# Performance work log

Hardware: AMD Instinct MI355X
Metric: run time of the kernel (lower is better)

## Reference

```python
import jax, jax.numpy as jnp
import numpy as np

EMBED_PHI = 1024
EMBED_F = 1024
HIDDEN_F = 1024
N_HEADS = 16
B, S = 2, 2048


def setup_inputs() -> dict:
    key = jax.random.key(0)
    ks = jax.random.split(key, 9)
    sphi = 1.0 / np.sqrt(EMBED_PHI)
    sf = 1.0 / np.sqrt(EMBED_F)
    sh = 1.0 / np.sqrt(HIDDEN_F)
    return {
        "q": jax.random.normal(ks[0], (B, S, EMBED_PHI), jnp.float32),
        "k": jax.random.normal(ks[1], (B, S, EMBED_PHI), jnp.float32),
        "v": jax.random.normal(ks[2], (B, S, EMBED_F), jnp.float32),
        "Wq": jax.random.normal(ks[3], (HIDDEN_F, EMBED_PHI), jnp.float32) * sphi,
        "Wk": jax.random.normal(ks[4], (HIDDEN_F, EMBED_PHI), jnp.float32) * sphi,
        "Wv": jax.random.normal(ks[5], (HIDDEN_F, EMBED_F), jnp.float32) * sf,
        "bv": jax.random.normal(ks[6], (HIDDEN_F,), jnp.float32) * sf,
        "Wo": jax.random.normal(ks[7], (EMBED_F, HIDDEN_F), jnp.float32) * sh,
        "bo": jax.random.normal(ks[8], (EMBED_F,), jnp.float32) * sh,
    }


def reference(q, k, v, Wq, Wk, Wv, bv, Wo, bo):
    Bq, Sq, _ = q.shape
    hd = HIDDEN_F // N_HEADS
    scale = 1.0 / np.sqrt(hd)
    # projections; torch Linear: y = x @ W.T + b
    qh = (q @ Wq.T).reshape(Bq, Sq, N_HEADS, hd).transpose(0, 2, 1, 3)  # [B,H,S,d]
    kh = (k @ Wk.T).reshape(Bq, Sq, N_HEADS, hd).transpose(0, 2, 1, 3)
    vh = (v @ Wv.T + bv).reshape(Bq, Sq, N_HEADS, hd).transpose(0, 2, 1, 3)
    scores = jnp.einsum("bhsd,bhtd->bhst", qh, kh) * scale  # [B,H,S,S]
    # mask: triu(diagonal=0) masked (attend strictly to past) except [0,0] unmasked
    mask = jnp.triu(jnp.ones((Sq, Sq), dtype=bool), k=0).at[0, 0].set(False)
    scores = jnp.where(mask, -jnp.inf, scores)
    probs = jax.nn.softmax(scores, axis=-1)  # dropout is identity at eval
    out = jnp.einsum("bhst,bhtd->bhsd", probs, vh)
    out = out.transpose(0, 2, 1, 3).reshape(Bq, Sq, HIDDEN_F)
    return out @ Wo.T + bo
```

## Files before the change

### kernel.cpp

```cpp
#include <hip/hip_runtime.h>
#include <hip/hip_bf16.h>

typedef __attribute__((ext_vector_type(8))) short short8;
typedef __attribute__((ext_vector_type(4))) float f32x4;

#define NE  1024
#define SEQ 2048

__device__ __forceinline__ float bf2f(unsigned short u) {
    union { unsigned u; float f; } x; x.u = ((unsigned)u) << 16; return x.f;
}
__device__ __forceinline__ unsigned short f2bf(float f) {
    union { float f; unsigned u; } x; x.f = f;
    unsigned r = x.u + 0x7FFFu + ((x.u >> 16) & 1u);
    return (unsigned short)(r >> 16);
}
__device__ __forceinline__ unsigned short f2bf_fast(float f) {
    union { float f; unsigned u; } x; x.f = f;
    return (unsigned short)((x.u + 0x8000u) >> 16);
}

__global__ void detect_dtype(const unsigned short* __restrict__ s,
                             int* __restrict__ flag) {
    __shared__ int cnt;
    const int t = threadIdx.x;
    if (t == 0) cnt = 0;
    __syncthreads();
    unsigned short u = s[t];
    int e = (u >> 7) & 0xFF;
    int sane = (e == 0) || (e >= 100 && e <= 140);
    atomicAdd(&cnt, sane);
    __syncthreads();
    if (t == 0) flag[0] = (cnt >= 230) ? 1 : 0;
}

struct Ptrs7 { const void* s[7]; unsigned short* d[7]; };

__global__ void convert7(Ptrs7 p, const int* __restrict__ flag, int zoff) {
    const int z = blockIdx.z + zoff;
    const int n = (z < 3) ? (4 << 20) : (1 << 20);
    const bool in_f32 = (flag[0] == 0);
    unsigned short* d = p.d[z];
    const int stride = gridDim.x * blockDim.x;
    for (int i8 = blockIdx.x * blockDim.x + threadIdx.x; i8 * 8 < n; i8 += stride) {
        size_t off = (size_t)i8 * 8;
        if (in_f32) {
            const float* sp = (const float*)p.s[z] + off;
            float4 a = *(const float4*)sp, b2 = *(const float4*)(sp + 4);
            short8 sv;
            sv[0] = (short)f2bf(a.x);  sv[1] = (short)f2bf(a.y);
            sv[2] = (short)f2bf(a.z);  sv[3] = (short)f2bf(a.w);
            sv[4] = (short)f2bf(b2.x); sv[5] = (short)f2bf(b2.y);
            sv[6] = (short)f2bf(b2.z); sv[7] = (short)f2bf(b2.w);
            *(short8*)(d + off) = sv;
        } else {
            *(short8*)(d + off) = *(const short8*)((const unsigned short*)p.s[z] + off);
        }
    }
}

template<int AWS, int WWS, int OUTF>
__global__ __launch_bounds__(256, 3)
void gemm_bt(const void* A0, const void* A1, const void* A2,
             const void* W0, const void* W1, const void* W2,
             const void* b0, const void* b1, const void* b2,
             void* C0, void* C1, void* C2,
             const int* __restrict__ flag)
{
    __shared__ __align__(16) unsigned short As[128 * 32];
    __shared__ __align__(16) unsigned short Bs[128 * 32];
    const int z = blockIdx.z;
    const void* Ap = (z == 0) ? A0 : (z == 1) ? A1 : A2;
    const void* Wp = (z == 0) ? W0 : (z == 1) ? W1 : W2;
    const void* bp = (z == 0) ? b0 : (z == 1) ? b1 : b2;
    void*       Cp = (z == 0) ? C0 : (z == 1) ? C1 : C2;
    const bool in_f32 = (flag[0] == 0);
    const int t = threadIdx.x;
    const int w = t >> 6, l = t & 63, q = l >> 4, n = l & 15;
    const int m0 = blockIdx.y * 128, n0 = blockIdx.x * 128;
    const int wm = (w >> 1) * 64, wn = (w & 1) * 64;
    const int srow = t >> 2, sk = (t & 3) * 8;

    f32x4 acc[4][4] = {};

    for (int k0 = 0; k0 < NE; k0 += 32) {
        if (AWS || !in_f32) {
            #pragma unroll
            for (int hh = 0; hh < 2; hh++) {
                const unsigned short* ga = (const unsigned short*)Ap +
                    (size_t)(m0 + srow + hh * 64) * NE + k0 + sk;
                __builtin_amdgcn_global_load_lds(
                    (const __attribute__((address_space(1))) void*)ga,
                    (__attribute__((address_space(3))) void*)&As[hh * 2048 + w * 512],
                    16, 0, 0);
            }
        } else {
            #pragma unroll
            for (int hh = 0; hh < 2; hh++) {
                const float* a = (const float*)Ap +
                                 (size_t)(m0 + srow + hh * 64) * NE + k0 + sk;
                float4 x0 = *(const float4*)a, x1 = *(const float4*)(a + 4);
                short8 sv;
                sv[0] = (short)f2bf(x0.x); sv[1] = (short)f2bf(x0.y);
                sv[2] = (short)f2bf(x0.z); sv[3] = (short)f2bf(x0.w);
                sv[4] = (short)f2bf(x1.x); sv[5] = (short)f2bf(x1.y);
                sv[6] = (short)f2bf(x1.z); sv[7] = (short)f2bf(x1.w);
                *(short8*)(&As[hh * 2048 + t * 8]) = sv;
            }
        }
        if (WWS || !in_f32) {
            #pragma unroll
            for (int hh = 0; hh < 2; hh++) {
                const unsigned short* ga = (const unsigned short*)Wp +
                    (size_t)(n0 + srow + hh * 64) * NE + k0 + sk;
                __builtin_amdgcn_global_load_lds(
                    (const __attribute__((address_space(1))) void*)ga,
                    (__attribute__((address_space(3))) void*)&Bs[hh * 2048 + w * 512],
                    16, 0, 0);
            }
        } else {
            #pragma unroll
            for (int hh = 0; hh < 2; hh++) {
                const float* a = (const float*)Wp +
                                 (size_t)(n0 + srow + hh * 64) * NE + k0 + sk;
                float4 x0 = *(const float4*)a, x1 = *(const float4*)(a + 4);
                short8 sv;
                sv[0] = (short)f2bf(x0.x); sv[1] = (short)f2bf(x0.y);
                sv[2] = (short)f2bf(x0.z); sv[3] = (short)f2bf(x0.w);
                sv[4] = (short)f2bf(x1.x); sv[5] = (short)f2bf(x1.y);
                sv[6] = (short)f2bf(x1.z); sv[7] = (short)f2bf(x1.w);
                *(short8*)(&Bs[hh * 2048 + t * 8]) = sv;
            }
        }
        __syncthreads();

        short8 af[4], bfv[4];
        #pragma unroll
        for (int mt = 0; mt < 4; mt++)
            af[mt] = *(const short8*)(&As[(wm + mt * 16 + n) * 32 + q * 8]);
        #pragma unroll
        for (int nt = 0; nt < 4; nt++)
            bfv[nt] = *(const short8*)(&Bs[(wn + nt * 16 + n) * 32 + q * 8]);
        #pragma unroll
        for (int mt = 0; mt < 4; mt++)
            #pragma unroll
            for (int nt = 0; nt < 4; nt++)
                acc[mt][nt] = __builtin_amdgcn_mfma_f32_16x16x32_bf16(
                    af[mt], bfv[nt], acc[mt][nt], 0, 0, 0);
        __syncthreads();
    }

    #pragma unroll
    for (int mt = 0; mt < 4; mt++)
        #pragma unroll
        for (int nt = 0; nt < 4; nt++)
            #pragma unroll
            for (int r = 0; r < 4; r++) {
                int row = m0 + wm + mt * 16 + q * 4 + r;
                int col = n0 + wn + nt * 16 + n;
                float v2 = acc[mt][nt][r];
                if (bp)
                    v2 += in_f32 ? ((const float*)bp)[col]
                                 : bf2f(((const unsigned short*)bp)[col]);
                size_t idx = (size_t)row * NE + col;
                if (OUTF && in_f32) ((float*)Cp)[idx] = v2;
                else                ((unsigned short*)Cp)[idx] = f2bf(v2);
            }
}

__global__ __launch_bounds__(128, 2)
void attn(const unsigned short* qh, const unsigned short* kh,
          const unsigned short* vh, unsigned short* ctx)
{
    __shared__ __align__(16) unsigned short Ks[64 * 72];
    __shared__ __align__(16) unsigned short Vt[64 * 72];
    __shared__ __align__(16) unsigned short Ps[2][2][16 * 72];
    const int t = threadIdx.x, w = t >> 6, l = t & 63;
    const int q = l >> 4, n = l & 15;
    const int bx = blockIdx.x;
    const int pair = bx & 15, rh = bx >> 4;
    const int qbB = pair, qbA = 31 - pair;
    const int h = blockIdx.y, b = blockIdx.z;
    const size_t base = (size_t)b * SEQ * NE + h * 64;
    const int rowoff = rh * 32 + w * 16;
    const int iA0 = qbA * 64 + rowoff, iB0 = qbB * 64 + rowoff;

    short8 qfA[2], qfB[2];
    qfA[0] = *(const short8*)(&qh[base + (size_t)(iA0 + n) * NE + q * 8]);
    qfA[1] = *(const short8*)(&qh[base + (size_t)(iA0 + n) * NE + 32 + q * 8]);
    qfB[0] = *(const short8*)(&qh[base + (size_t)(iB0 + n) * NE + q * 8]);
    qfB[1] = *(const short8*)(&qh[base + (size_t)(iB0 + n) * NE + 32 + q * 8]);

    f32x4 oA[4] = {}, oB[4] = {};
    float lA[4] = {0.f, 0.f, 0.f, 0.f}, lB[4] = {0.f, 0.f, 0.f, 0.f};

    const float K1 = 0.125f * 1.4426950408889634f;
    const float B2 = 24.0f * 1.4426950408889634f;

    short8 pkk[4], pv0[2], pv1[2];
    {
        #pragma unroll
        for (int i = 0; i < 4; i++) {
            int c = t + i * 128;
            pkk[i] = *(const short8*)(&kh[base + (size_t)(c >> 3) * NE + (c & 7) * 8]);
        }
        #pragma unroll
        for (int i = 0; i < 2; i++) {
            int u = t + i * 128;
            int j2 = (u & 31) * 2, d8 = (u >> 5) * 8;
            pv0[i] = *(const short8*)(&vh[base + (size_t)j2 * NE + d8]);
            pv1[i] = *(const short8*)(&vh[base + (size_t)(j2 + 1) * NE + d8]);
        }
    }

    for (int jt = 0; jt <= qbA; jt++) {
        #pragma unroll
        for (int i = 0; i < 4; i++) {
            int c = t + i * 128;
            *(short8*)(&Ks[(c >> 3) * 72 + (c & 7) * 8]) = pkk[i];
        }
        #pragma unroll
        for (int i = 0; i < 2; i++) {
            int u = t + i * 128;
            int j2 = (u & 31) * 2, d8 = (u >> 5) * 8;
            #pragma unroll
            for (int e = 0; e < 8; e++) {
                unsigned pkd = (unsigned)(unsigned short)pv0[i][e] |
                               ((unsigned)(unsigned short)pv1[i][e] << 16);
                *(unsigned*)(&Vt[(d8 + e) * 72 + j2]) = pkd;
            }
        }
        __syncthreads();

        if (jt < qbA) {
            const int jn = jt + 1;
            #pragma unroll
            for (int i = 0; i < 4; i++) {
                int c = t + i * 128;
                pkk[i] = *(const short8*)(&kh[base + (size_t)(jn * 64 + (c >> 3)) * NE + (c & 7) * 8]);
            }
            #pragma unroll
            for (int i = 0; i < 2; i++) {
                int u = t + i * 128;
                int j2 = (u & 31) * 2, d8 = (u >> 5) * 8;
                pv0[i] = *(const short8*)(&vh[base + (size_t)(jn * 64 + j2) * NE + d8]);
                pv1[i] = *(const short8*)(&vh[base + (size_t)(jn * 64 + j2 + 1) * NE + d8]);
            }
        }

        #pragma unroll
        for (int half = 0; half < 2; half++) {
            if (half == 1 && jt > qbB) break;
            const short8* qf = half ? qfB : qfA;
            f32x4* o = half ? oB : oA;
            float* ls = half ? lB : lA;
            const int i0 = half ? iB0 : iA0;
            const int qbS = half ? qbB : qbA;
            unsigned short* PsW = &Ps[w][half][0];

            f32x4 sa[4] = {};
            #pragma unroll
            for (int ks = 0; ks < 2; ks++)
                #pragma unroll
                for (int nt = 0; nt < 4; nt++) {
                    short8 kf = *(const short8*)(&Ks[(nt * 16 + n) * 72 + ks * 32 + q * 8]);
                    sa[nt] = __builtin_amdgcn_mfma_f32_16x16x32_bf16(qf[ks], kf, sa[nt], 0, 0, 0);
                }

            const bool diag = (jt == qbS);
            #pragma unroll
            for (int nt = 0; nt < 4; nt++)
                #pragma unroll
                for (int r = 0; r < 4; r++) {
                    float e = fmaf(sa[nt][r], K1, -B2);
                    if (diag) {
                        int j = jt * 64 + nt * 16 + n;
                        int i = i0 + q * 4 + r;
                        bool ok = (j < i) || (i == 0 && j == 0);
                        e = ok ? e : -256.0f;
                    }
                    float p = __builtin_amdgcn_exp2f(e);
                    ls[r] += p;
                    PsW[(q * 4 + r) * 72 + nt * 16 + n] = f2bf_fast(p);
                }
            asm volatile("s_waitcnt lgkmcnt(0)" ::: "memory");

            #pragma unroll
            for (int ks = 0; ks < 2; ks++) {
                short8 pf = *(const short8*)(&PsW[n * 72 + ks * 32 + q * 8]);
                #pragma unroll
                for (int dt = 0; dt < 4; dt++) {
                    short8 vf = *(const short8*)(&Vt[(dt * 16 + n) * 72 + ks * 32 + q * 8]);
                    o[dt] = __builtin_amdgcn_mfma_f32_16x16x32_bf16(pf, vf, o[dt], 0, 0, 0);
                }
            }
        }
        __syncthreads();
    }

    #pragma unroll
    for (int r = 0; r < 4; r++) {
        #pragma unroll
        for (int xm = 1; xm <= 8; xm <<= 1) {
            lA[r] += __shfl_xor(lA[r], xm, 64);
            lB[r] += __shfl_xor(lB[r], xm, 64);
        }
    }
    #pragma unroll
    for (int r = 0; r < 4; r++) {
        float invA = 1.0f / lA[r], invB = 1.0f / lB[r];
        #pragma unroll
        for (int dt = 0; dt < 4; dt++) {
            ctx[base + (size_t)(iA0 + q * 4 + r) * NE + dt * 16 + n] = f2bf(oA[dt][r] * invA);
            ctx[base + (size_t)(iB0 + q * 4 + r) * NE + dt * 16 + n] = f2bf(oB[dt][r] * invB);
        }
    }
}

extern "C" void kernel_launch(void* const* d_in, const int* in_sizes, int n_in,
                              void* d_out, int out_size, void* d_ws, size_t ws_size,
                              hipStream_t stream) {
    const void* q  = d_in[0];
    const void* k  = d_in[1];
    const void* v  = d_in[2];
    const void* Wq = d_in[3];
    const void* Wk = d_in[4];
    const void* Wv = d_in[5];
    const void* bv = d_in[6];
    const void* Wo = d_in[7];
    const void* bo = d_in[8];

    const size_t MB = 1024 * 1024;
    const size_t M4 = 4 * MB;
    unsigned short* ws = (unsigned short*)d_ws;
    unsigned short* qh  = ws;
    unsigned short* kh  = ws + 1 * M4;
    unsigned short* vh  = ws + 2 * M4;
    unsigned short* ctx = qh;

    int tier = (ws_size >= 56 * MB + 64) ? 2 : (ws_size >= 32 * MB + 64) ? 1 : 0;

    unsigned short *qc, *kc, *vc, *Wqc, *Wkc, *Wvc, *Woc;
    int* flag;
    if (tier == 2) {
        qc = ws + 3 * M4; kc = ws + 4 * M4; vc = ws + 5 * M4;
        Wqc = ws + 6 * M4;           Wkc = Wqc + 1 * MB;
        Wvc = Wqc + 2 * MB;          Woc = Wqc + 3 * MB;
        flag = (int*)((char*)d_ws + 56 * MB);
    } else if (tier == 1) {
        qc = kc = vc = nullptr;
        Wqc = ws + 3 * M4;           Wkc = Wqc + 1 * MB;
        Wvc = Wqc + 2 * MB;          Woc = Wqc + 3 * MB;
        flag = (int*)((char*)d_ws + 32 * MB);
    } else {
        qc = kc = vc = nullptr; Wqc = Wkc = Wvc = Woc = nullptr;
        flag = (int*)((char*)d_ws + 24 * MB);
    }

    detect_dtype<<<1, 256, 0, stream>>>((const unsigned short*)q, flag);

    if (tier > 0) {
        Ptrs7 p;
        p.s[0] = q;  p.s[1] = k;  p.s[2] = v;
        p.s[3] = Wq; p.s[4] = Wk; p.s[5] = Wv; p.s[6] = Wo;
        p.d[0] = qc; p.d[1] = kc; p.d[2] = vc;
        p.d[3] = Wqc; p.d[4] = Wkc; p.d[5] = Wvc; p.d[6] = Woc;
        if (tier == 2)
            convert7<<<dim3(512, 1, 7), 256, 0, stream>>>(p, flag, 0);
        else
            convert7<<<dim3(512, 1, 4), 256, 0, stream>>>(p, flag, 3);
    }

    if (tier == 2)
        gemm_bt<1, 1, 0><<<dim3(8, 32, 3), 256, 0, stream>>>(
            qc, kc, vc, Wqc, Wkc, Wvc, nullptr, nullptr, bv, qh, kh, vh, flag);
    else if (tier == 1)
        gemm_bt<0, 1, 0><<<dim3(8, 32, 3), 256, 0, stream>>>(
            q, k, v, Wqc, Wkc, Wvc, nullptr, nullptr, bv, qh, kh, vh, flag);
    else
        gemm_bt<0, 0, 0><<<dim3(8, 32, 3), 256, 0, stream>>>(
            q, k, v, Wq, Wk, Wv, nullptr, nullptr, bv, qh, kh, vh, flag);

    attn<<<dim3(32, 16, 2), 128, 0, stream>>>(qh, kh, vh, ctx);

    if (tier > 0)
        gemm_bt<1, 1, 1><<<dim3(8, 32, 1), 256, 0, stream>>>(
            ctx, ctx, ctx, Woc, Woc, Woc, bo, bo, bo, d_out, d_out, d_out, flag);
    else
        gemm_bt<1, 0, 1><<<dim3(8, 32, 1), 256, 0, stream>>>(
            ctx, ctx, ctx, Wo, Wo, Wo, bo, bo, bo, d_out, d_out, d_out, flag);
}
```

Before: 252.1 us.

## Merge paired attention blocks into one 512-thread block sharing K/V tiles

The attention kernel now launches 16x16x2 blocks of 512 threads instead of 32x16x2 blocks of 128. Each block covers both paired query tiles (A and B) fully, one warp per 16 query rows. The point is to load each K/V tile into shared memory once for twice as many query rows, halving global K/V traffic and the staging work per warp. In exchange, the warps on the short B tile sit idle at barriers once jt passes qbB. The grid also drops to 512 larger blocks, which lowers block-level parallelism.

New measurement: 242.0 us. 1.04x faster.

```diff
diff --git a/kernel.cpp b/kernel.cpp
--- a/kernel.cpp
+++ b/kernel.cpp
@@ -168,96 +168,67 @@
             }
 }
 
-__global__ __launch_bounds__(128, 2)
+__global__ __launch_bounds__(512, 4)
 void attn(const unsigned short* qh, const unsigned short* kh,
           const unsigned short* vh, unsigned short* ctx)
 {
     __shared__ __align__(16) unsigned short Ks[64 * 72];
     __shared__ __align__(16) unsigned short Vt[64 * 72];
-    __shared__ __align__(16) unsigned short Ps[2][2][16 * 72];
+    __shared__ __align__(16) unsigned short Ps[8][16 * 72];
     const int t = threadIdx.x, w = t >> 6, l = t & 63;
     const int q = l >> 4, n = l & 15;
-    const int bx = blockIdx.x;
-    const int pair = bx & 15, rh = bx >> 4;
+    const int half = w >> 2, sub = w & 3;
+    const int pair = blockIdx.x;
     const int qbB = pair, qbA = 31 - pair;
+    const int qb = half ? qbB : qbA;
     const int h = blockIdx.y, b = blockIdx.z;
     const size_t base = (size_t)b * SEQ * NE + h * 64;
-    const int rowoff = rh * 32 + w * 16;
-    const int iA0 = qbA * 64 + rowoff, iB0 = qbB * 64 + rowoff;
-
-    short8 qfA[2], qfB[2];
-    qfA[0] = *(const short8*)(&qh[base + (size_t)(iA0 + n) * NE + q * 8]);
-    qfA[1] = *(const short8*)(&qh[base + (size_t)(iA0 + n) * NE + 32 + q * 8]);
-    qfB[0] = *(const short8*)(&qh[base + (size_t)(iB0 + n) * NE + q * 8]);
-    qfB[1] = *(const short8*)(&qh[base + (size_t)(iB0 + n) * NE + 32 + q * 8]);
-
-    f32x4 oA[4] = {}, oB[4] = {};
-    float lA[4] = {0.f, 0.f, 0.f, 0.f}, lB[4] = {0.f, 0.f, 0.f, 0.f};
+    const int i0 = qb * 64 + sub * 16;
+
+    short8 qf[2];
+    qf[0] = *(const short8*)(&qh[base + (size_t)(i0 + n) * NE + q * 8]);
+    qf[1] = *(const short8*)(&qh[base + (size_t)(i0 + n) * NE + 32 + q * 8]);
+
+    f32x4 o[4] = {};
+    float ls[4] = {0.f, 0.f, 0.f, 0.f};
 
     const float K1 = 0.125f * 1.4426950408889634f;
     const float B2 = 24.0f * 1.4426950408889634f;
 
-    short8 pkk[4], pv0[2], pv1[2];
-    {
-        #pragma unroll
-        for (int i = 0; i < 4; i++) {
-            int c = t + i * 128;
-            pkk[i] = *(const short8*)(&kh[base + (size_t)(c >> 3) * NE + (c & 7) * 8]);
-        }
-        #pragma unroll
-        for (int i = 0; i < 2; i++) {
-            int u = t + i * 128;
-            int j2 = (u & 31) * 2, d8 = (u >> 5) * 8;
-            pv0[i] = *(const short8*)(&vh[base + (size_t)j2 * NE + d8]);
-            pv1[i] = *(const short8*)(&vh[base + (size_t)(j2 + 1) * NE + d8]);
-        }
-    }
+    const int kr = t >> 3, kc = (t & 7) * 8;
+    const int j2 = (t & 31) * 2, d8 = ((t >> 5) & 7) * 8;
+
+    short8 pk, pv0, pv1;
+    pk = *(const short8*)(&kh[base + (size_t)kr * NE + kc]);
+    if (t < 256) {
+        pv0 = *(const short8*)(&vh[base + (size_t)j2 * NE + d8]);
+        pv1 = *(const short8*)(&vh[base + (size_t)(j2 + 1) * NE + d8]);
+    }
+
+    unsigned short* PsW = &Ps[w][0];
 
     for (int jt = 0; jt <= qbA; jt++) {
-        #pragma unroll
-        for (int i = 0; i < 4; i++) {
-            int c = t + i * 128;
-            *(short8*)(&Ks[(c >> 3) * 72 + (c & 7) * 8]) = pkk[i];
-        }
-        #pragma unroll
-        for (int i = 0; i < 2; i++) {
-            int u = t + i * 128;
-            int j2 = (u & 31) * 2, d8 = (u >> 5) * 8;
+        *(short8*)(&Ks[kr * 72 + kc]) = pk;
+        if (t < 256) {
             #pragma unroll
             for (int e = 0; e < 8; e++) {
-                unsigned pkd = (unsigned)(unsigned short)pv0[i][e] |
-                               ((unsigned)(unsigned short)pv1[i][e] << 16);
+                unsigned pkd = (unsigned)(unsigned short)pv0[e] |
+                               ((unsigned)(unsigned short)pv1[e] << 16);
                 *(unsigned*)(&Vt[(d8 + e) * 72 + j2]) = pkd;
             }
         }
         __syncthreads();
 
         if (jt < qbA) {
-            const int jn = jt + 1;
-            #pragma unroll
-            for (int i = 0; i < 4; i++) {
-                int c = t + i * 128;
-                pkk[i] = *(const short8*)(&kh[base + (size_t)(jn * 64 + (c >> 3)) * NE + (c & 7) * 8]);
-            }
-            #pragma unroll
-            for (int i = 0; i < 2; i++) {
-                int u = t + i * 128;
-                int j2 = (u & 31) * 2, d8 = (u >> 5) * 8;
-                pv0[i] = *(const short8*)(&vh[base + (size_t)(jn * 64 + j2) * NE + d8]);
-                pv1[i] = *(const short8*)(&vh[base + (size_t)(jn * 64 + j2 + 1) * NE + d8]);
-            }
-        }
-
-        #pragma unroll
-        for (int half = 0; half < 2; half++) {
-            if (half == 1 && jt > qbB) break;
-            const short8* qf = half ? qfB : qfA;
-            f32x4* o = half ? oB : oA;
-            float* ls = half ? lB : lA;
-            const int i0 = half ? iB0 : iA0;
-            const int qbS = half ? qbB : qbA;
-            unsigned short* PsW = &Ps[w][half][0];
-
+            const int jn = (jt + 1) * 64;
+            pk = *(const short8*)(&kh[base + (size_t)(jn + kr) * NE + kc]);
+            if (t < 256) {
+                pv0 = *(const short8*)(&vh[base + (size_t)(jn + j2) * NE + d8]);
+                pv1 = *(const short8*)(&vh[base + (size_t)(jn + j2 + 1) * NE + d8]);
+            }
+        }
+
+        if (jt <= qb) {
             f32x4 sa[4] = {};
             #pragma unroll
             for (int ks = 0; ks < 2; ks++)
@@ -267,7 +238,7 @@
                     sa[nt] = __builtin_amdgcn_mfma_f32_16x16x32_bf16(qf[ks], kf, sa[nt], 0, 0, 0);
                 }
 
-            const bool diag = (jt == qbS);
+            const bool diag = (jt == qb);
             #pragma unroll
             for (int nt = 0; nt < 4; nt++)
                 #pragma unroll
@@ -299,21 +270,18 @@
     }
 
     #pragma unroll
-    for (int r = 0; r < 4; r++) {
-        #pragma unroll
-        for (int xm = 1; xm <= 8; xm <<= 1) {
-            lA[r] += __shfl_xor(lA[r], xm, 64);
-            lB[r] += __shfl_xor(lB[r], xm, 64);
-        }
-    }
+    for (int r = 0; r < 4; r++)
+        #pragma unroll
+        for (int xm = 1; xm <= 8; xm <<= 1)
+            ls[r] += __shfl_xor(ls[r], xm, 64);
+
     #pragma unroll
     for (int r = 0; r < 4; r++) {
-        float invA = 1.0f / lA[r], invB = 1.0f / lB[r];
-        #pragma unroll
-        for (int dt = 0; dt < 4; dt++) {
-            ctx[base + (size_t)(iA0 + q * 4 + r) * NE + dt * 16 + n] = f2bf(oA[dt][r] * invA);
-            ctx[base + (size_t)(iB0 + q * 4 + r) * NE + dt * 16 + n] = f2bf(oB[dt][r] * invB);
-        }
+        float inv = 1.0f / ls[r];
+        #pragma unroll
+        for (int dt = 0; dt < 4; dt++)
+            ctx[base + (size_t)(i0 + q * 4 + r) * NE + dt * 16 + n] =
+                f2bf(o[dt][r] * inv);
     }
 }
 
@@ -381,7 +349,7 @@
         gemm_bt<0, 0, 0><<<dim3(8, 32, 3), 256, 0, stream>>>(
             q, k, v, Wq, Wk, Wv, nullptr, nullptr, bv, qh, kh, vh, flag);
 
-    attn<<<dim3(32, 16, 2), 128, 0, stream>>>(qh, kh, vh, ctx);
+    attn<<<dim3(16, 16, 2), 512, 0, stream>>>(qh, kh, vh, ctx);
 
     if (tier > 0)
         gemm_bt<1, 1, 1><<<dim3(8, 32, 1), 256, 0, stream>>>(
```
